# Performance work log

Hardware: AMD Instinct MI355X
Metric: run time of the kernel (lower is better)

The kernel has to match this reference:

```python
import math
import jax, jax.numpy as jnp
import numpy as np

N_HEADS = 16


def setup_inputs() -> dict:
    key = jax.random.key(0)
    qkv = jax.random.normal(key, (4, 3072, 2048), dtype=jnp.float32)
    return {"qkv": qkv}


def reference(qkv) -> jnp.ndarray:
    bs, width, length = qkv.shape
    assert width % (3 * N_HEADS) == 0
    ch = width // (3 * N_HEADS)
    # [bs*H, 3*ch, T] -> q, k, v each [bs*H, ch, T]
    qkv_r = qkv.reshape(bs * N_HEADS, 3 * ch, length)
    q, k, v = qkv_r[:, :ch], qkv_r[:, ch:2 * ch], qkv_r[:, 2 * ch:]
    scale = 1.0 / math.sqrt(math.sqrt(ch))
    # scores: [bs*H, T, T]
    weight = jnp.einsum('bct,bcs->bts', q * scale, k * scale)
    weight = jax.nn.softmax(weight.astype(jnp.float32), axis=-1).astype(weight.dtype)
    a = jnp.einsum('bts,bcs->bct', weight, v)  # [bs*H, ch, T]
    return a.reshape(bs, N_HEADS * ch, length)
```

## Files before the change

### kernel.cpp

```cpp
#include <hip/hip_runtime.h>
#include <hip/hip_bf16.h>
#include <cstdint>
#include <cstddef>

typedef short bf16x8 __attribute__((ext_vector_type(8)));
typedef float f32x4 __attribute__((ext_vector_type(4)));
typedef float f32x16 __attribute__((ext_vector_type(16)));

#if __has_builtin(__builtin_amdgcn_exp2f)
#define EXP2F(x) __builtin_amdgcn_exp2f(x)
#else
#define EXP2F(x) exp2f(x)
#endif

#define QSCALE 0.18033688011112043f

__device__ __forceinline__ short f2bf(float f) {
  union { __hip_bfloat16 b; short s; } u;
  u.b = __float2bfloat16(f);
  return u.s;
}

__device__ __forceinline__ unsigned int bitsf(float f) {
  union { float f; unsigned int u; } x; x.f = f; return x.u;
}

__device__ __forceinline__ unsigned int pkbf(float a, float b) {
  return ((bitsf(a) + 0x8000u) >> 16) | ((bitsf(b) + 0x8000u) & 0xFFFF0000u);
}

__global__ __launch_bounds__(256, 4) void qkv_prep_kernel(
    const float* __restrict__ qkv, short* __restrict__ Kt,
    short* __restrict__ Vb) {
  const int bh = blockIdx.x >> 5;
  const int s0 = (blockIdx.x & 31) << 6;
  const int tid = threadIdx.x;
  const int row = tid >> 2;
  const int part = tid & 3;
  __shared__ float lds[64 * 65];

  const size_t qb = (size_t)bh * (192 * 2048);

  {
    const float* src = qkv + qb + (size_t)(64 + row) * 2048 + s0 + part * 16;
#pragma unroll
    for (int k4 = 0; k4 < 4; ++k4) {
      float4 v = ((const float4*)src)[k4];
      float* p = &lds[row * 65 + part * 16 + k4 * 4];
      p[0] = v.x; p[1] = v.y; p[2] = v.z; p[3] = v.w;
    }
  }
  __syncthreads();
  {
    bf16x8 o0, o1;
#pragma unroll
    for (int k = 0; k < 8; ++k) o0[k] = f2bf(lds[(part * 16 + k) * 65 + row]);
#pragma unroll
    for (int k = 0; k < 8; ++k) o1[k] = f2bf(lds[(part * 16 + 8 + k) * 65 + row]);
    short* dst = Kt + ((size_t)bh * 2048 + s0 + row) * 64 + part * 16;
    *(bf16x8*)dst = o0;
    *(bf16x8*)(dst + 8) = o1;
  }
  {
    const float* src = qkv + qb + (size_t)(128 + row) * 2048 + s0 + part * 16;
    float a[16];
#pragma unroll
    for (int k4 = 0; k4 < 4; ++k4) {
      float4 v = ((const float4*)src)[k4];
      a[k4 * 4 + 0] = v.x; a[k4 * 4 + 1] = v.y;
      a[k4 * 4 + 2] = v.z; a[k4 * 4 + 3] = v.w;
    }
    bf16x8 o0, o1;
#pragma unroll
    for (int k = 0; k < 8; ++k) { o0[k] = f2bf(a[k]); o1[k] = f2bf(a[8 + k]); }
    short* dst = Vb + ((size_t)bh * 64 + row) * 2048 + s0 + part * 16;
    *(bf16x8*)dst = o0;
    *(bf16x8*)(dst + 8) = o1;
  }
}

__global__ __launch_bounds__(256, 3) void attn32_kernel(
    const float* __restrict__ qkv, const short* __restrict__ Kt,
    const short* __restrict__ Vb, float* __restrict__ out) {
  const int bid = blockIdx.x;
  const int vid = (bid & 7) * 128 + (bid >> 3);
  const int bh = vid >> 4;
  const int tblk = vid & 15;
  const int tid = threadIdx.x;
  const int wv = tid >> 6;
  const int lane = tid & 63;
  const int tl = lane & 31;
  const int hi = lane >> 5;
  const int t0w = tblk * 128 + wv * 32;

  __shared__ __align__(16) char smem[32768];

  const size_t qb = (size_t)bh * (192 * 2048);
  bf16x8 qf[4];
#pragma unroll
  for (int kc = 0; kc < 4; ++kc) {
#pragma unroll
    for (int j = 0; j < 8; ++j) {
      const int c = kc * 16 + hi * 8 + j;
      qf[kc][j] = f2bf(qkv[qb + (size_t)c * 2048 + t0w + tl] * QSCALE);
    }
  }

  f32x16 acc[2];
#pragma unroll
  for (int cb = 0; cb < 2; ++cb)
#pragma unroll
    for (int r = 0; r < 16; ++r) acc[cb][r] = 0.f;

  float mrun = -1e30f;
  float lsum = 0.f;

  const int srow = tid >> 3;
  const int col8 = tid & 7;
  const short* kptr = Kt + (size_t)bh * (2048 * 64) + (size_t)srow * 64 + col8 * 8;
  const short* vptr = Vb + ((size_t)bh * 64 + srow) * 2048 + col8 * 8;
  const int sdst = srow * 128 + ((col8 * 16) ^ ((srow & 7) * 16));

  bf16x8 kq[2], vq[2];
#pragma unroll
  for (int q = 0; q < 2; ++q) {
    kq[q] = *(const bf16x8*)(kptr + (size_t)(q * 32) * 64);
    vq[q] = *(const bf16x8*)(vptr + (size_t)(q * 32) * 2048);
  }

  for (int ch = 0; ch < 32; ++ch) {
    char* const Kls = smem + (ch & 1) * 16384;
    char* const Vls = Kls + 8192;

#pragma unroll
    for (int q = 0; q < 2; ++q) {
      *(bf16x8*)(Kls + sdst + q * 4096) = kq[q];
      *(bf16x8*)(Vls + sdst + q * 4096) = vq[q];
    }
    __syncthreads();

    const int s0n = (ch < 31 ? ch + 1 : 31) * 64;
    bf16x8 kn[2], vn[2];
#pragma unroll
    for (int q = 0; q < 2; ++q) {
      kn[q] = *(const bf16x8*)(kptr + (size_t)(s0n + q * 32) * 64);
      vn[q] = *(const bf16x8*)(vptr + (size_t)(q * 32) * 2048 + s0n);
    }

    f32x16 lg[2];
#pragma unroll
    for (int st = 0; st < 2; ++st) {
#pragma unroll
      for (int r = 0; r < 16; ++r) lg[st][r] = 0.f;
      const int row = st * 32 + tl;
      const int rsw = (row & 7) * 16;
#pragma unroll
      for (int kc = 0; kc < 4; ++kc) {
        const bf16x8 ka =
            *(const bf16x8*)(Kls + row * 128 + ((kc * 32 + hi * 16) ^ rsw));
        lg[st] = __builtin_amdgcn_mfma_f32_32x32x16_bf16(ka, qf[kc], lg[st],
                                                         0, 0, 0);
      }
    }

    float cm = fmaxf(lg[0][0], lg[1][0]);
#pragma unroll
    for (int r = 1; r < 16; ++r) cm = fmaxf(cm, fmaxf(lg[0][r], lg[1][r]));
    cm = fmaxf(cm, __shfl_xor(cm, 32));
    if (!__all(cm <= mrun + 8.0f)) {
      const float nm = fmaxf(mrun, cm);
      const float fac = EXP2F(mrun - nm);
      mrun = nm;
      lsum *= fac;
#pragma unroll
      for (int cb = 0; cb < 2; ++cb)
#pragma unroll
        for (int r = 0; r < 16; ++r) acc[cb][r] *= fac;
    }

#pragma unroll
    for (int st = 0; st < 2; ++st)
#pragma unroll
      for (int r = 0; r < 16; ++r) {
        lg[st][r] = EXP2F(lg[st][r] - mrun);
        lsum += lg[st][r];
      }

    bf16x8 pa[4];
#pragma unroll
    for (int st = 0; st < 2; ++st) {
#pragma unroll
      for (int kl = 0; kl < 2; ++kl) {
        const unsigned int p0a = pkbf(lg[st][8 * kl + 0], lg[st][8 * kl + 1]);
        const unsigned int p0b = pkbf(lg[st][8 * kl + 2], lg[st][8 * kl + 3]);
        const unsigned int p1a = pkbf(lg[st][8 * kl + 4], lg[st][8 * kl + 5]);
        const unsigned int p1b = pkbf(lg[st][8 * kl + 6], lg[st][8 * kl + 7]);
        const unsigned int sa = hi ? p0a : p1a;
        const unsigned int sb = hi ? p0b : p1b;
        const unsigned int ra = __shfl_xor(sa, 32);
        const unsigned int rb = __shfl_xor(sb, 32);
        union { unsigned int w[4]; bf16x8 v; } u;
        u.w[0] = hi ? ra : p0a;
        u.w[1] = hi ? rb : p0b;
        u.w[2] = hi ? p1a : ra;
        u.w[3] = hi ? p1b : rb;
        pa[st * 2 + kl] = u.v;
      }
    }

#pragma unroll
    for (int cb = 0; cb < 2; ++cb) {
      const int rowv = cb * 32 + tl;
      const int vsw = (rowv & 7) * 16;
#pragma unroll
      for (int ks = 0; ks < 4; ++ks) {
        const bf16x8 vb =
            *(const bf16x8*)(Vls + rowv * 128 + ((ks * 32 + hi * 16) ^ vsw));
        acc[cb] = __builtin_amdgcn_mfma_f32_32x32x16_bf16(vb, pa[ks], acc[cb],
                                                          0, 0, 0);
      }
    }

#pragma unroll
    for (int q = 0; q < 2; ++q) { kq[q] = kn[q]; vq[q] = vn[q]; }
  }

  const float ls = lsum + __shfl_xor(lsum, 32);
  const float inv = 1.0f / ls;
#pragma unroll
  for (int cb = 0; cb < 2; ++cb) {
#pragma unroll
    for (int r = 0; r < 16; ++r) {
      const int c = cb * 32 + (r & 3) + 8 * (r >> 2) + 4 * hi;
      out[((size_t)bh * 64 + c) * 2048 + t0w + tl] = acc[cb][r] * inv;
    }
  }
}

extern "C" void kernel_launch(void* const* d_in, const int* in_sizes, int n_in,
                              void* d_out, int out_size, void* d_ws,
                              size_t ws_size, hipStream_t stream) {
  (void)in_sizes; (void)n_in; (void)out_size;
  const float* qkv = (const float*)d_in[0];
  float* out = (float*)d_out;
  const size_t kv_elems = (size_t)64 * 2048 * 64;
  if (ws_size < kv_elems * 2 * sizeof(short)) return;
  short* Kt = (short*)d_ws;
  short* Vb = Kt + kv_elems;
  hipLaunchKernelGGL(qkv_prep_kernel, dim3(2048), dim3(256), 0, stream,
                     qkv, Kt, Vb);
  hipLaunchKernelGGL(attn32_kernel, dim3(1024), dim3(256), 0, stream,
                     qkv, Kt, Vb, out);
}
```

Measured before the change: 129.5 us.

## Stage K/V tiles via direct global-to-LDS loads and raise occupancy

```diff
diff --git a/kernel.cpp b/kernel.cpp
--- a/kernel.cpp
+++ b/kernel.cpp
@@ -4,7 +4,6 @@
 #include <cstddef>
 
 typedef short bf16x8 __attribute__((ext_vector_type(8)));
-typedef float f32x4 __attribute__((ext_vector_type(4)));
 typedef float f32x16 __attribute__((ext_vector_type(16)));
 
 #if __has_builtin(__builtin_amdgcn_exp2f)
@@ -21,12 +20,17 @@
   return u.s;
 }
 
-__device__ __forceinline__ unsigned int bitsf(float f) {
-  union { float f; unsigned int u; } x; x.f = f; return x.u;
-}
-
-__device__ __forceinline__ unsigned int pkbf(float a, float b) {
-  return ((bitsf(a) + 0x8000u) >> 16) | ((bitsf(b) + 0x8000u) & 0xFFFF0000u);
+__device__ __forceinline__ unsigned int packbf2(float a, float b) {
+  union { unsigned short u[2]; unsigned int w; } x;
+  x.u[0] = (unsigned short)f2bf(a);
+  x.u[1] = (unsigned short)f2bf(b);
+  return x.w;
+}
+
+__device__ __forceinline__ void gload16(const short* g, char* l) {
+  __builtin_amdgcn_global_load_lds(
+      (const __attribute__((address_space(1))) void*)g,
+      (__attribute__((address_space(3))) void*)l, 16, 0, 0);
 }
 
 __global__ __launch_bounds__(256, 4) void qkv_prep_kernel(
@@ -79,7 +83,7 @@
   }
 }
 
-__global__ __launch_bounds__(256, 3) void attn32_kernel(
+__global__ __launch_bounds__(256, 4) void attn32_kernel(
     const float* __restrict__ qkv, const short* __restrict__ Kt,
     const short* __restrict__ Vb, float* __restrict__ out) {
   const int bid = blockIdx.x;
@@ -115,36 +119,43 @@
   float mrun = -1e30f;
   float lsum = 0.f;
 
-  const int srow = tid >> 3;
-  const int col8 = tid & 7;
-  const short* kptr = Kt + (size_t)bh * (2048 * 64) + (size_t)srow * 64 + col8 * 8;
-  const short* vptr = Vb + ((size_t)bh * 64 + srow) * 2048 + col8 * 8;
-  const int sdst = srow * 128 + ((col8 * 16) ^ ((srow & 7) * 16));
-
-  bf16x8 kq[2], vq[2];
-#pragma unroll
-  for (int q = 0; q < 2; ++q) {
-    kq[q] = *(const bf16x8*)(kptr + (size_t)(q * 32) * 64);
-    vq[q] = *(const bf16x8*)(vptr + (size_t)(q * 32) * 2048);
-  }
-
+  const int r8 = lane >> 3;
+  const int sl = lane & 7;
+  const int row0 = wv * 16 + r8;
+  const int row1 = wv * 16 + 8 + r8;
+  const short* kg0 = Kt + (size_t)bh * (2048 * 64) + (size_t)row0 * 64 +
+                     ((sl ^ (row0 & 7)) * 8);
+  const short* kg1 = Kt + (size_t)bh * (2048 * 64) + (size_t)row1 * 64 +
+                     ((sl ^ (row1 & 7)) * 8);
+  const short* vg0 = Vb + ((size_t)bh * 64 + row0) * 2048 +
+                     ((sl ^ (row0 & 7)) * 8);
+  const short* vg1 = Vb + ((size_t)bh * 64 + row1) * 2048 +
+                     ((sl ^ (row1 & 7)) * 8);
+  const int ldK0 = (wv * 16) * 128;
+  const int ldK1 = (wv * 16 + 8) * 128;
+
+  {
+    gload16(kg0, smem + ldK0);
+    gload16(kg1, smem + ldK1);
+    gload16(vg0, smem + 8192 + ldK0);
+    gload16(vg1, smem + 8192 + ldK1);
+  }
+
+#pragma unroll 2
   for (int ch = 0; ch < 32; ++ch) {
     char* const Kls = smem + (ch & 1) * 16384;
     char* const Vls = Kls + 8192;
 
-#pragma unroll
-    for (int q = 0; q < 2; ++q) {
-      *(bf16x8*)(Kls + sdst + q * 4096) = kq[q];
-      *(bf16x8*)(Vls + sdst + q * 4096) = vq[q];
-    }
     __syncthreads();
 
-    const int s0n = (ch < 31 ? ch + 1 : 31) * 64;
-    bf16x8 kn[2], vn[2];
-#pragma unroll
-    for (int q = 0; q < 2; ++q) {
-      kn[q] = *(const bf16x8*)(kptr + (size_t)(s0n + q * 32) * 64);
-      vn[q] = *(const bf16x8*)(vptr + (size_t)(q * 32) * 2048 + s0n);
+    if (ch < 31) {
+      char* const Knx = smem + ((ch + 1) & 1) * 16384;
+      const size_t ka = (size_t)(ch + 1) * 4096;
+      const int va = (ch + 1) * 64;
+      gload16(kg0 + ka, Knx + ldK0);
+      gload16(kg1 + ka, Knx + ldK1);
+      gload16(vg0 + va, Knx + 8192 + ldK0);
+      gload16(vg1 + va, Knx + 8192 + ldK1);
     }
 
     f32x16 lg[2];
@@ -163,10 +174,15 @@
       }
     }
 
-    float cm = fmaxf(lg[0][0], lg[1][0]);
-#pragma unroll
-    for (int r = 1; r < 16; ++r) cm = fmaxf(cm, fmaxf(lg[0][r], lg[1][r]));
-    cm = fmaxf(cm, __shfl_xor(cm, 32));
+    float mt[16];
+#pragma unroll
+    for (int r = 0; r < 16; ++r) mt[r] = fmaxf(lg[0][r], lg[1][r]);
+#pragma unroll
+    for (int s = 8; s >= 1; s >>= 1)
+#pragma unroll
+      for (int r = 0; r < 8; ++r)
+        if (r < s) mt[r] = fmaxf(mt[r], mt[r + s]);
+    float cm = fmaxf(mt[0], __shfl_xor(mt[0], 32));
     if (!__all(cm <= mrun + 8.0f)) {
       const float nm = fmaxf(mrun, cm);
       const float fac = EXP2F(mrun - nm);
@@ -178,23 +194,25 @@
         for (int r = 0; r < 16; ++r) acc[cb][r] *= fac;
     }
 
-#pragma unroll
-    for (int st = 0; st < 2; ++st)
-#pragma unroll
-      for (int r = 0; r < 16; ++r) {
-        lg[st][r] = EXP2F(lg[st][r] - mrun);
-        lsum += lg[st][r];
-      }
+    float ps = 0.f;
+#pragma unroll
+    for (int st = 0; st < 2; ++st) {
+#pragma unroll
+      for (int r = 0; r < 16; ++r) lg[st][r] = EXP2F(lg[st][r] - mrun);
+#pragma unroll
+      for (int r = 0; r < 8; ++r) ps += lg[st][2 * r] + lg[st][2 * r + 1];
+    }
+    lsum += ps;
 
     bf16x8 pa[4];
 #pragma unroll
     for (int st = 0; st < 2; ++st) {
 #pragma unroll
       for (int kl = 0; kl < 2; ++kl) {
-        const unsigned int p0a = pkbf(lg[st][8 * kl + 0], lg[st][8 * kl + 1]);
-        const unsigned int p0b = pkbf(lg[st][8 * kl + 2], lg[st][8 * kl + 3]);
-        const unsigned int p1a = pkbf(lg[st][8 * kl + 4], lg[st][8 * kl + 5]);
-        const unsigned int p1b = pkbf(lg[st][8 * kl + 6], lg[st][8 * kl + 7]);
+        const unsigned int p0a = packbf2(lg[st][8 * kl + 0], lg[st][8 * kl + 1]);
+        const unsigned int p0b = packbf2(lg[st][8 * kl + 2], lg[st][8 * kl + 3]);
+        const unsigned int p1a = packbf2(lg[st][8 * kl + 4], lg[st][8 * kl + 5]);
+        const unsigned int p1b = packbf2(lg[st][8 * kl + 6], lg[st][8 * kl + 7]);
         const unsigned int sa = hi ? p0a : p1a;
         const unsigned int sb = hi ? p0b : p1b;
         const unsigned int ra = __shfl_xor(sa, 32);
@@ -220,9 +238,6 @@
                                                           0, 0, 0);
       }
     }
-
-#pragma unroll
-    for (int q = 0; q < 2; ++q) { kq[q] = kn[q]; vq[q] = vn[q]; }
   }
 
   const float ls = lsum + __shfl_xor(lsum, 32);
```

Result: faster. 125.5 us (-3.1%).
